# Performance work log

Hardware: AMD Instinct MI355X
Metric: run time of the kernel (lower is better)

The kernel has to match this reference:

```python
import jax, jax.numpy as jnp
import numpy as np

DIM = 512
NUM_HEADS = 8
HEAD_DIM = DIM // NUM_HEADS
REL_POS_BINS = 961
B, N = 64, 256


def setup_inputs() -> dict:
    key = jax.random.key(0)
    ks = jax.random.split(key, 7)
    x = jax.random.normal(ks[0], (B, N, DIM), dtype=jnp.float32)
    rel_pos_index = jax.random.randint(ks[1], (N, N), 0, REL_POS_BINS)
    s = 1.0 / np.sqrt(DIM)
    qkv_w = jax.random.normal(ks[2], (3 * DIM, DIM), dtype=jnp.float32) * s
    qkv_b = jax.random.normal(ks[3], (3 * DIM,), dtype=jnp.float32) * 0.02
    proj_w = jax.random.normal(ks[4], (DIM, DIM), dtype=jnp.float32) * s
    proj_b = jax.random.normal(ks[5], (DIM,), dtype=jnp.float32) * 0.02
    rel_pos_bias = jax.random.normal(ks[6], (NUM_HEADS, REL_POS_BINS), dtype=jnp.float32) * 0.02
    return {"x": x, "rel_pos_index": rel_pos_index, "qkv_w": qkv_w,
            "qkv_b": qkv_b, "proj_w": proj_w, "proj_b": proj_b,
            "rel_pos_bias": rel_pos_bias}


def reference(x, rel_pos_index, qkv_w, qkv_b, proj_w, proj_b, rel_pos_bias):
    Bn, Nn, C = x.shape
    H, D = NUM_HEADS, HEAD_DIM
    qkv = x @ qkv_w.T + qkv_b                      # (B,N,3C)
    qkv = qkv.reshape(Bn, Nn, 3, H, D).transpose(2, 0, 3, 1, 4)  # (3,B,H,N,D)
    q, k, v = qkv[0], qkv[1], qkv[2]
    scale = 1.0 / jnp.sqrt(jnp.asarray(D, dtype=x.dtype))
    scores = jnp.einsum('bhnd,bhmd->bhnm', q, k) * scale          # (B,H,N,N)
    bias = rel_pos_bias[:, rel_pos_index]                          # (H,N,N) gather
    scores = scores + bias[None]
    attn = jax.nn.softmax(scores, axis=-1)
    out = jnp.einsum('bhnm,bhmd->bhnd', attn, v)                   # (B,H,N,D)
    out = out.transpose(0, 2, 1, 3).reshape(Bn, Nn, C)
    return out @ proj_w.T + proj_b
```

## Files before the change

### kernel.cpp

```cpp
#include <hip/hip_runtime.h>
#include <stdint.h>

#define DIM 512
#define NHEADS 8
#define HDIM 64
#define NBINS 961
#define BATCH 64
#define SEQ 256
#define NTOK (BATCH*SEQ)
#define BHND (BATCH*NHEADS*SEQ*HDIM)

using bf16x8 = __attribute__((ext_vector_type(8))) short;
using f32x4  = __attribute__((ext_vector_type(4))) float;

__device__ __forceinline__ unsigned short f2bf(float f) {
  unsigned u = __float_as_uint(f);
  u += 0x7FFF + ((u >> 16) & 1);
  return (unsigned short)(u >> 16);
}

__device__ __forceinline__ void async16(const void* g, void* lds) {
  __builtin_amdgcn_global_load_lds(
      (const __attribute__((address_space(1))) unsigned int*)g,
      (__attribute__((address_space(3))) unsigned int*)lds,
      16, 0, 0);
}


__global__ void cast_kernel(const float* __restrict__ in,
                            unsigned short* __restrict__ out, int n4) {
  int i = blockIdx.x * 256 + threadIdx.x;
  if (i >= n4) return;
  float4 f = reinterpret_cast<const float4*>(in)[i];
  ushort4 o;
  o.x = f2bf(f.x); o.y = f2bf(f.y); o.z = f2bf(f.z); o.w = f2bf(f.w);
  reinterpret_cast<ushort4*>(out)[i] = o;
}

__global__ void bias_kernel(const int* __restrict__ idx,
                            const float* __restrict__ rpb,
                            float* __restrict__ bf) {
  int i = blockIdx.x * 256 + threadIdx.x;
  if (i >= NHEADS * SEQ * SEQ) return;
  int h = i >> 16;
  int r = i & 65535;
  int n = r >> 8, m = r & 255;
  bf[(size_t)h * 65536 + n * 256 + (m & 15) * 16 + (m >> 4)] = rpb[h * NBINS + idx[r]];
}


__device__ __forceinline__ void stage_tile(const unsigned short* __restrict__ A,
                                           const unsigned short* __restrict__ Bw,
                                           char* slot, int T,
                                           int m0, int n0, int t) {
  const int kk = T * 32;
  const int wv64 = (t >> 6) << 6;
#pragma unroll
  for (int i = 0; i < 2; ++i) {
    int c = t + i * 256;
    int row = c >> 2, ch = c & 3;
    int sch = ch ^ ((row >> 1) & 3);
    const unsigned short* ga = A + (size_t)(m0 + row) * 512 + kk + sch * 8;
    async16(ga, slot + (i * 256 + wv64) * 16);
    const unsigned short* gb = Bw + (size_t)(n0 + row) * 512 + kk + sch * 8;
    async16(gb, slot + 8192 + (i * 256 + wv64) * 16);
  }
}

template<int EPI>
__global__ __launch_bounds__(256, 3) void gemm_bt(
    const unsigned short* __restrict__ A,
    const unsigned short* __restrict__ Bw,
    const float* __restrict__ bias,
    void* __restrict__ outp) {
  __shared__ char gsm[49152];
  const int t = threadIdx.x;
  const int lane = t & 63;
  const int l15 = lane & 15, lg = lane >> 4;
  const int m0 = blockIdx.x * 128, n0 = blockIdx.y * 128;
  const int wv = t >> 6;
  const int wm = wv & 1, wn = wv >> 1;

  f32x4 acc[4][4];
  const f32x4 fz = {0.f, 0.f, 0.f, 0.f};
#pragma unroll
  for (int a = 0; a < 4; ++a)
#pragma unroll
    for (int b = 0; b < 4; ++b) acc[a][b] = fz;

  stage_tile(A, Bw, gsm,         0, m0, n0, t);
  stage_tile(A, Bw, gsm + 16384, 1, m0, n0, t);

  int cur = 0;
#pragma unroll 1
  for (int T = 0; T < 16; ++T) {
    if (T < 15) asm volatile("s_waitcnt vmcnt(4)" ::: "memory");
    else        asm volatile("s_waitcnt vmcnt(0)" ::: "memory");
    __builtin_amdgcn_s_barrier();
    __builtin_amdgcn_sched_barrier(0);

    if (T < 14) {
      int dst = cur + 2; if (dst >= 3) dst -= 3;
      stage_tile(A, Bw, gsm + dst * 16384, T + 2, m0, n0, t);
    }
    __builtin_amdgcn_sched_barrier(0);

    char* As = gsm + cur * 16384;
    char* Bs = As + 8192;
    bf16x8 af[4], bfr[4];
#pragma unroll
    for (int x = 0; x < 4; ++x) {
      int ra = wm * 64 + x * 16 + l15;
      af[x]  = *(const bf16x8*)(As + ra * 64 + ((lg ^ ((ra >> 1) & 3)) * 16));
      int rb = wn * 64 + x * 16 + l15;
      bfr[x] = *(const bf16x8*)(Bs + rb * 64 + ((lg ^ ((rb >> 1) & 3)) * 16));
    }
    asm volatile("s_waitcnt lgkmcnt(0)" ::: "memory");
    __builtin_amdgcn_sched_barrier(0);

    __builtin_amdgcn_s_setprio(1);
#pragma unroll
    for (int mi = 0; mi < 4; ++mi)
#pragma unroll
      for (int ni = 0; ni < 4; ++ni)
        acc[mi][ni] = __builtin_amdgcn_mfma_f32_16x16x32_bf16(af[mi], bfr[ni], acc[mi][ni], 0, 0, 0);
    __builtin_amdgcn_s_setprio(0);

    cur = cur + 1; if (cur >= 3) cur -= 3;
  }

#pragma unroll
  for (int mi = 0; mi < 4; ++mi)
#pragma unroll
    for (int ni = 0; ni < 4; ++ni)
#pragma unroll
      for (int r = 0; r < 4; ++r) {
        int row = m0 + wm * 64 + mi * 16 + lg * 4 + r;
        int col = n0 + wn * 64 + ni * 16 + l15;
        float v = acc[mi][ni][r] + bias[col];
        if (EPI == 0) {
          int which = col >> 9, hd = col & 511;
          int b = row >> 8, n = row & 255;
          ((unsigned short*)outp)[(size_t)which * BHND +
              (((size_t)(b * NHEADS + (hd >> 6)) * SEQ + n) * HDIM) + (hd & 63)] = f2bf(v);
        } else {
          ((float*)outp)[(size_t)row * 512 + col] = v;
        }
      }
}


__global__ __launch_bounds__(512, 2) void attn_kernel(
    const unsigned short* __restrict__ qb,
    const unsigned short* __restrict__ kb,
    const unsigned short* __restrict__ vb,
    const float* __restrict__ biasf,
    unsigned short* __restrict__ aout) {
  extern __shared__ char smem[];
  char* k_s = smem;
  char* v_s = smem + 32768;
  const int t = threadIdx.x, lane = t & 63, w = t >> 6;
  const int l15 = lane & 15, lg = lane >> 4;
  char* P_s = smem + w * 4096;
  const int bh = blockIdx.x;
  const int h = bh & 7;
  const int b = bh >> 3;
  const size_t base = (size_t)bh * (SEQ * HDIM);

#pragma unroll
  for (int i = 0; i < 4; ++i) {
    int c = i * 512 + t;
    int row = c >> 3, sl = c & 7;
    bf16x8 val = *(const bf16x8*)(kb + base + (size_t)c * 8);
    *(bf16x8*)(k_s + row * 128 + ((sl * 16) ^ ((row & 7) << 4))) = val;
  }
#pragma unroll
  for (int i = 0; i < 4; ++i) {
    int c = i * 512 + t;
    int key = c >> 3, d0 = (c & 7) * 8;
    bf16x8 val = *(const bf16x8*)(vb + base + (size_t)c * 8);
#pragma unroll
    for (int j = 0; j < 8; ++j) {
      int d = d0 + j;
      int term = (((d & 7) ^ ((d >> 3) & 7)) << 4);
      *(short*)(v_s + d * 512 + ((key * 2) ^ term)) = val[j];
    }
  }
  bf16x8 qa[2][2];
#pragma unroll
  for (int rf = 0; rf < 2; ++rf)
#pragma unroll
    for (int ks = 0; ks < 2; ++ks)
      qa[rf][ks] = *(const bf16x8*)(qb + base + (size_t)(w * 32 + rf * 16 + l15) * 64 + ks * 32 + lg * 8);
  __syncthreads();

  f32x4 accs[2][16];
  const f32x4 fz = {0.f, 0.f, 0.f, 0.f};
#pragma unroll
  for (int a = 0; a < 2; ++a)
#pragma unroll
    for (int c = 0; c < 16; ++c) accs[a][c] = fz;
  __builtin_amdgcn_s_setprio(1);
#pragma unroll
  for (int cf = 0; cf < 16; ++cf) {
    int key = cf * 16 + l15;
#pragma unroll
    for (int ks = 0; ks < 2; ++ks) {
      bf16x8 kf = *(const bf16x8*)(k_s + key * 128 + ((lg * 16 + ks * 64) ^ ((key & 7) << 4)));
      accs[0][cf] = __builtin_amdgcn_mfma_f32_16x16x32_bf16(qa[0][ks], kf, accs[0][cf], 0, 0, 0);
      accs[1][cf] = __builtin_amdgcn_mfma_f32_16x16x32_bf16(qa[1][ks], kf, accs[1][cf], 0, 0, 0);
    }
  }
  __builtin_amdgcn_s_setprio(0);

  const float* bh_ptr = biasf + (size_t)h * 65536;
#pragma unroll
  for (int rf = 0; rf < 2; ++rf)
#pragma unroll
    for (int r = 0; r < 4; ++r) {
      int n = w * 32 + rf * 16 + lg * 4 + r;
      const f32x4* bp = (const f32x4*)(bh_ptr + n * 256 + l15 * 16);
      f32x4 b0 = bp[0], b1 = bp[1], b2 = bp[2], b3 = bp[3];
#pragma unroll
      for (int cf = 0; cf < 16; ++cf) {
        float bb = (cf < 4) ? b0[cf] : (cf < 8) ? b1[cf - 4] : (cf < 12) ? b2[cf - 8] : b3[cf - 12];
        accs[rf][cf][r] = accs[rf][cf][r] * 0.125f + bb;
      }
    }

  float pinv[2][4];
#pragma unroll
  for (int rf = 0; rf < 2; ++rf)
#pragma unroll
    for (int r = 0; r < 4; ++r) {
      float m = -1e30f;
#pragma unroll
      for (int cf = 0; cf < 16; ++cf) m = fmaxf(m, accs[rf][cf][r]);
#pragma unroll
      for (int off = 1; off < 16; off <<= 1) m = fmaxf(m, __shfl_xor(m, off, 64));
      float s = 0.f;
#pragma unroll
      for (int cf = 0; cf < 16; ++cf) {
        float p = __expf(accs[rf][cf][r] - m);
        accs[rf][cf][r] = p;
        s += p;
      }
#pragma unroll
      for (int off = 1; off < 16; off <<= 1) s += __shfl_xor(s, off, 64);
      pinv[rf][r] = 1.0f / s;
    }

  __syncthreads();

  f32x4 acco[2][4];
#pragma unroll
  for (int a = 0; a < 2; ++a)
#pragma unroll
    for (int c2 = 0; c2 < 4; ++c2) acco[a][c2] = fz;

  for (int ch = 0; ch < 4; ++ch) {
#pragma unroll
    for (int rf = 0; rf < 2; ++rf)
#pragma unroll
      for (int cl = 0; cl < 4; ++cl)
#pragma unroll
        for (int r = 0; r < 4; ++r) {
          int rowl = rf * 16 + lg * 4 + r;
          int ml = cl * 16 + l15;
          float p = accs[rf][ch * 4 + cl][r] * pinv[rf][r];
          *(short*)(P_s + rowl * 128 + ((ml * 2) ^ ((rowl & 7) << 4))) = (short)f2bf(p);
        }
#pragma unroll
    for (int ks = 0; ks < 2; ++ks) {
      bf16x8 pa[2];
#pragma unroll
      for (int rf = 0; rf < 2; ++rf) {
        int row = rf * 16 + l15;
        pa[rf] = *(const bf16x8*)(P_s + row * 128 + ((lg * 16 + ks * 64) ^ ((row & 7) << 4)));
      }
      int keyb = (ch * 64 + ks * 32 + lg * 8) * 2;
      __builtin_amdgcn_s_setprio(1);
#pragma unroll
      for (int df = 0; df < 4; ++df) {
        int d = df * 16 + l15;
        int term = (((d & 7) ^ ((d >> 3) & 7)) << 4);
        bf16x8 vf = *(const bf16x8*)(v_s + d * 512 + (keyb ^ term));
        acco[0][df] = __builtin_amdgcn_mfma_f32_16x16x32_bf16(pa[0], vf, acco[0][df], 0, 0, 0);
        acco[1][df] = __builtin_amdgcn_mfma_f32_16x16x32_bf16(pa[1], vf, acco[1][df], 0, 0, 0);
      }
      __builtin_amdgcn_s_setprio(0);
    }
  }

#pragma unroll
  for (int rf = 0; rf < 2; ++rf)
#pragma unroll
    for (int df = 0; df < 4; ++df)
#pragma unroll
      for (int r = 0; r < 4; ++r) {
        int n = w * 32 + rf * 16 + lg * 4 + r;
        int d = df * 16 + l15;
        aout[((size_t)(b * SEQ + n)) * DIM + h * HDIM + d] = f2bf(acco[rf][df][r]);
      }
}


extern "C" void kernel_launch(void* const* d_in, const int* in_sizes, int n_in,
                              void* d_out, int out_size, void* d_ws, size_t ws_size,
                              hipStream_t stream) {
  const float* x      = (const float*)d_in[0];
  const int*   rpi    = (const int*)d_in[1];
  const float* qkv_w  = (const float*)d_in[2];
  const float* qkv_b  = (const float*)d_in[3];
  const float* proj_w = (const float*)d_in[4];
  const float* proj_b = (const float*)d_in[5];
  const float* rpb    = (const float*)d_in[6];

  char* ws = (char*)d_ws;
  unsigned short* xb    = (unsigned short*)ws;
  unsigned short* wqkv  = (unsigned short*)(ws + 16777216);
  unsigned short* wproj = (unsigned short*)(ws + 18350080);
  float*          biasf = (float*)         (ws + 18874368);
  unsigned short* qkvb  = (unsigned short*)(ws + 20971520);
  unsigned short* aoutb = (unsigned short*)(ws + 71303168);

  cast_kernel<<<8192, 256, 0, stream>>>(x, xb, 2097152);
  cast_kernel<<<768, 256, 0, stream>>>(qkv_w, wqkv, 196608);
  cast_kernel<<<256, 256, 0, stream>>>(proj_w, wproj, 65536);
  bias_kernel<<<2048, 256, 0, stream>>>(rpi, rpb, biasf);

  dim3 g1(128, 12);
  gemm_bt<0><<<g1, 256, 0, stream>>>(xb, wqkv, qkv_b, (void*)qkvb);

  attn_kernel<<<512, 512, 65536, stream>>>(qkvb, qkvb + BHND, qkvb + 2 * (size_t)BHND,
                                           biasf, aoutb);

  dim3 g2(128, 4);
  gemm_bt<1><<<g2, 256, 0, stream>>>(aoutb, wproj, proj_b, d_out);
}
```

Baseline: 110.5 us.

## Use 256-row 8-wave GEMM tiles and split attention per query quarter

The GEMM moves to 512-thread blocks with 256xBN tiles, a 64-wide K step with double buffering, staging of B spread across MFMA phases, and a blockIdx remap that groups neighbouring tiles per XCD. The goal is more operand reuse per LDS load and better L2 locality. Attention now runs one block per quarter of the query rows (256 threads, 2048 blocks) to raise parallelism and cut registers per wave. The cost is that each block reloads the full K and V for its head, four times the K/V staging traffic, and the GEMM needs a large LDS allocation that may limit occupancy.

```diff
diff --git a/kernel.cpp b/kernel.cpp
--- a/kernel.cpp
+++ b/kernel.cpp
@@ -49,95 +49,102 @@
 }
 
 
-__device__ __forceinline__ void stage_tile(const unsigned short* __restrict__ A,
-                                           const unsigned short* __restrict__ Bw,
-                                           char* slot, int T,
-                                           int m0, int n0, int t) {
-  const int kk = T * 32;
-  const int wv64 = (t >> 6) << 6;
+__device__ __forceinline__ void stage_half(const unsigned short* __restrict__ X,
+                                           int row0, int kk, char* dst, int t) {
 #pragma unroll
   for (int i = 0; i < 2; ++i) {
-    int c = t + i * 256;
-    int row = c >> 2, ch = c & 3;
-    int sch = ch ^ ((row >> 1) & 3);
-    const unsigned short* ga = A + (size_t)(m0 + row) * 512 + kk + sch * 8;
-    async16(ga, slot + (i * 256 + wv64) * 16);
-    const unsigned short* gb = Bw + (size_t)(n0 + row) * 512 + kk + sch * 8;
-    async16(gb, slot + 8192 + (i * 256 + wv64) * 16);
-  }
-}
-
-template<int EPI>
-__global__ __launch_bounds__(256, 3) void gemm_bt(
+    int q = i * 512 + t;
+    int r = q >> 3, s = q & 7;
+    const unsigned short* src = X + (size_t)(row0 + r) * 512 + kk + ((s ^ (r & 7)) << 3);
+    async16(src, dst + (size_t)(i * 512 + ((t >> 6) << 6)) * 16);
+  }
+}
+
+template<int NBW, int EPI>
+__global__ __launch_bounds__(512) void gemm8p(
     const unsigned short* __restrict__ A,
     const unsigned short* __restrict__ Bw,
     const float* __restrict__ bias,
-    void* __restrict__ outp) {
-  __shared__ char gsm[49152];
+    void* __restrict__ outp, int nbn, int cpx) {
+  extern __shared__ char gsm[];
+  constexpr int BN   = NBW * 64;
+  constexpr int BUF  = 32768 + NBW * 8192;
   const int t = threadIdx.x;
-  const int lane = t & 63;
-  const int l15 = lane & 15, lg = lane >> 4;
-  const int m0 = blockIdx.x * 128, n0 = blockIdx.y * 128;
-  const int wv = t >> 6;
-  const int wm = wv & 1, wn = wv >> 1;
-
-  f32x4 acc[4][4];
+  const int lane = t & 63, l15 = lane & 15, lg = lane >> 4;
+  const int wv = t >> 6, wm = wv & 1, wn = wv >> 1;
+  const int bid = blockIdx.x;
+  const int nid = (bid & 7) * cpx + (bid >> 3);
+  const int m0 = (nid / nbn) * 256, n0 = (nid % nbn) * BN;
+
+  f32x4 acc[8][NBW];
   const f32x4 fz = {0.f, 0.f, 0.f, 0.f};
 #pragma unroll
-  for (int a = 0; a < 4; ++a)
-#pragma unroll
-    for (int b = 0; b < 4; ++b) acc[a][b] = fz;
-
-  stage_tile(A, Bw, gsm,         0, m0, n0, t);
-  stage_tile(A, Bw, gsm + 16384, 1, m0, n0, t);
+  for (int a = 0; a < 8; ++a)
+#pragma unroll
+    for (int b = 0; b < NBW; ++b) acc[a][b] = fz;
+
+  stage_half(A,  m0,       0, gsm,          t);
+  stage_half(A,  m0 + 128, 0, gsm + 16384,  t);
+  stage_half(Bw, n0,       0, gsm + 32768,  t);
+  if (NBW == 4) stage_half(Bw, n0 + 128, 0, gsm + 49152, t);
 
   int cur = 0;
 #pragma unroll 1
-  for (int T = 0; T < 16; ++T) {
-    if (T < 15) asm volatile("s_waitcnt vmcnt(4)" ::: "memory");
-    else        asm volatile("s_waitcnt vmcnt(0)" ::: "memory");
+  for (int T = 0; T < 8; ++T) {
+    char* Ab  = gsm + cur * BUF;
+    char* Bb  = Ab + 32768;
+    char* nxt = gsm + (cur ^ 1) * BUF;
+
     __builtin_amdgcn_s_barrier();
+    if (T < 7) {
+      stage_half(A, m0,       (T + 1) * 64, nxt,         t);
+      stage_half(A, m0 + 128, (T + 1) * 64, nxt + 16384, t);
+      asm volatile("s_waitcnt vmcnt(4)" ::: "memory");
+    } else {
+      asm volatile("s_waitcnt vmcnt(0)" ::: "memory");
+    }
     __builtin_amdgcn_sched_barrier(0);
 
-    if (T < 14) {
-      int dst = cur + 2; if (dst >= 3) dst -= 3;
-      stage_tile(A, Bw, gsm + dst * 16384, T + 2, m0, n0, t);
-    }
-    __builtin_amdgcn_sched_barrier(0);
-
-    char* As = gsm + cur * 16384;
-    char* Bs = As + 8192;
-    bf16x8 af[4], bfr[4];
-#pragma unroll
-    for (int x = 0; x < 4; ++x) {
-      int ra = wm * 64 + x * 16 + l15;
-      af[x]  = *(const bf16x8*)(As + ra * 64 + ((lg ^ ((ra >> 1) & 3)) * 16));
-      int rb = wn * 64 + x * 16 + l15;
-      bfr[x] = *(const bf16x8*)(Bs + rb * 64 + ((lg ^ ((rb >> 1) & 3)) * 16));
-    }
-    asm volatile("s_waitcnt lgkmcnt(0)" ::: "memory");
-    __builtin_amdgcn_sched_barrier(0);
-
-    __builtin_amdgcn_s_setprio(1);
-#pragma unroll
-    for (int mi = 0; mi < 4; ++mi)
-#pragma unroll
-      for (int ni = 0; ni < 4; ++ni)
-        acc[mi][ni] = __builtin_amdgcn_mfma_f32_16x16x32_bf16(af[mi], bfr[ni], acc[mi][ni], 0, 0, 0);
-    __builtin_amdgcn_s_setprio(0);
-
-    cur = cur + 1; if (cur >= 3) cur -= 3;
-  }
-
-#pragma unroll
-  for (int mi = 0; mi < 4; ++mi)
-#pragma unroll
-    for (int ni = 0; ni < 4; ++ni)
+#pragma unroll
+    for (int ph = 0; ph < 4; ++ph) {
+      const int kh = ph >> 1, mh = ph & 1;
+      if (ph == 1 && T < 7) stage_half(Bw, n0, (T + 1) * 64, nxt + 32768, t);
+      if (NBW == 4 && ph == 2 && T < 7) stage_half(Bw, n0 + 128, (T + 1) * 64, nxt + 49152, t);
+
+      const int sw = ((kh * 4 + lg) ^ (l15 & 7)) * 16;
+      bf16x8 av[4], bv[NBW];
+#pragma unroll
+      for (int mi = 0; mi < 4; ++mi)
+        av[mi] = *(const bf16x8*)(Ab + wm * 16384 + (mh * 64 + mi * 16 + l15) * 128 + sw);
+#pragma unroll
+      for (int ni = 0; ni < NBW; ++ni) {
+        int rb = wn * (NBW * 16) + ni * 16 + l15;
+        bv[ni] = *(const bf16x8*)(Bb + (rb >> 7) * 16384 + (rb & 127) * 128 + sw);
+      }
+      asm volatile("s_waitcnt lgkmcnt(0)" ::: "memory");
+      __builtin_amdgcn_sched_barrier(0);
+      __builtin_amdgcn_s_setprio(1);
+#pragma unroll
+      for (int mi = 0; mi < 4; ++mi)
+#pragma unroll
+        for (int ni = 0; ni < NBW; ++ni)
+          acc[mh * 4 + mi][ni] =
+              __builtin_amdgcn_mfma_f32_16x16x32_bf16(av[mi], bv[ni], acc[mh * 4 + mi][ni], 0, 0, 0);
+      __builtin_amdgcn_s_setprio(0);
+      __builtin_amdgcn_sched_barrier(0);
+    }
+    cur ^= 1;
+  }
+
+#pragma unroll
+  for (int MI = 0; MI < 8; ++MI)
+#pragma unroll
+    for (int ni = 0; ni < NBW; ++ni)
 #pragma unroll
       for (int r = 0; r < 4; ++r) {
-        int row = m0 + wm * 64 + mi * 16 + lg * 4 + r;
-        int col = n0 + wn * 64 + ni * 16 + l15;
-        float v = acc[mi][ni][r] + bias[col];
+        int row = m0 + wm * 128 + MI * 16 + lg * 4 + r;
+        int col = n0 + wn * (NBW * 16) + ni * 16 + l15;
+        float v = acc[MI][ni][r] + bias[col];
         if (EPI == 0) {
           int which = col >> 9, hd = col & 511;
           int b = row >> 8, n = row & 255;
@@ -150,7 +157,7 @@
 }
 
 
-__global__ __launch_bounds__(512, 2) void attn_kernel(
+__global__ __launch_bounds__(256) void attn_kernel(
     const unsigned short* __restrict__ qb,
     const unsigned short* __restrict__ kb,
     const unsigned short* __restrict__ vb,
@@ -161,22 +168,24 @@
   char* v_s = smem + 32768;
   const int t = threadIdx.x, lane = t & 63, w = t >> 6;
   const int l15 = lane & 15, lg = lane >> 4;
-  char* P_s = smem + w * 4096;
-  const int bh = blockIdx.x;
+  char* P_s = smem + w * 2048;
+  const int nid = (blockIdx.x & 7) * 256 + (blockIdx.x >> 3);
+  const int bh = nid >> 2, quarter = nid & 3;
   const int h = bh & 7;
   const int b = bh >> 3;
+  const int row0 = quarter * 64 + w * 16;
   const size_t base = (size_t)bh * (SEQ * HDIM);
 
 #pragma unroll
-  for (int i = 0; i < 4; ++i) {
-    int c = i * 512 + t;
+  for (int i = 0; i < 8; ++i) {
+    int c = i * 256 + t;
     int row = c >> 3, sl = c & 7;
     bf16x8 val = *(const bf16x8*)(kb + base + (size_t)c * 8);
     *(bf16x8*)(k_s + row * 128 + ((sl * 16) ^ ((row & 7) << 4))) = val;
   }
 #pragma unroll
-  for (int i = 0; i < 4; ++i) {
-    int c = i * 512 + t;
+  for (int i = 0; i < 8; ++i) {
+    int c = i * 256 + t;
     int key = c >> 3, d0 = (c & 7) * 8;
     bf16x8 val = *(const bf16x8*)(vb + base + (size_t)c * 8);
 #pragma unroll
@@ -186,20 +195,16 @@
       *(short*)(v_s + d * 512 + ((key * 2) ^ term)) = val[j];
     }
   }
-  bf16x8 qa[2][2];
-#pragma unroll
-  for (int rf = 0; rf < 2; ++rf)
-#pragma unroll
-    for (int ks = 0; ks < 2; ++ks)
-      qa[rf][ks] = *(const bf16x8*)(qb + base + (size_t)(w * 32 + rf * 16 + l15) * 64 + ks * 32 + lg * 8);
+  bf16x8 qa[2];
+#pragma unroll
+  for (int ks = 0; ks < 2; ++ks)
+    qa[ks] = *(const bf16x8*)(qb + base + (size_t)(row0 + l15) * 64 + ks * 32 + lg * 8);
   __syncthreads();
 
-  f32x4 accs[2][16];
+  f32x4 accs[16];
   const f32x4 fz = {0.f, 0.f, 0.f, 0.f};
 #pragma unroll
-  for (int a = 0; a < 2; ++a)
-#pragma unroll
-    for (int c = 0; c < 16; ++c) accs[a][c] = fz;
+  for (int c = 0; c < 16; ++c) accs[c] = fz;
   __builtin_amdgcn_s_setprio(1);
 #pragma unroll
   for (int cf = 0; cf < 16; ++cf) {
@@ -207,77 +212,63 @@
 #pragma unroll
     for (int ks = 0; ks < 2; ++ks) {
       bf16x8 kf = *(const bf16x8*)(k_s + key * 128 + ((lg * 16 + ks * 64) ^ ((key & 7) << 4)));
-      accs[0][cf] = __builtin_amdgcn_mfma_f32_16x16x32_bf16(qa[0][ks], kf, accs[0][cf], 0, 0, 0);
-      accs[1][cf] = __builtin_amdgcn_mfma_f32_16x16x32_bf16(qa[1][ks], kf, accs[1][cf], 0, 0, 0);
+      accs[cf] = __builtin_amdgcn_mfma_f32_16x16x32_bf16(qa[ks], kf, accs[cf], 0, 0, 0);
     }
   }
   __builtin_amdgcn_s_setprio(0);
 
   const float* bh_ptr = biasf + (size_t)h * 65536;
 #pragma unroll
-  for (int rf = 0; rf < 2; ++rf)
-#pragma unroll
-    for (int r = 0; r < 4; ++r) {
-      int n = w * 32 + rf * 16 + lg * 4 + r;
-      const f32x4* bp = (const f32x4*)(bh_ptr + n * 256 + l15 * 16);
-      f32x4 b0 = bp[0], b1 = bp[1], b2 = bp[2], b3 = bp[3];
-#pragma unroll
-      for (int cf = 0; cf < 16; ++cf) {
-        float bb = (cf < 4) ? b0[cf] : (cf < 8) ? b1[cf - 4] : (cf < 12) ? b2[cf - 8] : b3[cf - 12];
-        accs[rf][cf][r] = accs[rf][cf][r] * 0.125f + bb;
+  for (int r = 0; r < 4; ++r) {
+    int n = row0 + lg * 4 + r;
+    const f32x4* bp = (const f32x4*)(bh_ptr + n * 256 + l15 * 16);
+    f32x4 b0 = bp[0], b1 = bp[1], b2 = bp[2], b3 = bp[3];
+#pragma unroll
+    for (int cf = 0; cf < 16; ++cf) {
+      float bb = (cf < 4) ? b0[cf] : (cf < 8) ? b1[cf - 4] : (cf < 12) ? b2[cf - 8] : b3[cf - 12];
+      accs[cf][r] = accs[cf][r] * 0.125f + bb;
+    }
+  }
+
+  float pinv[4];
+#pragma unroll
+  for (int r = 0; r < 4; ++r) {
+    float m = -1e30f;
+#pragma unroll
+    for (int cf = 0; cf < 16; ++cf) m = fmaxf(m, accs[cf][r]);
+#pragma unroll
+    for (int off = 1; off < 16; off <<= 1) m = fmaxf(m, __shfl_xor(m, off, 64));
+    float s = 0.f;
+#pragma unroll
+    for (int cf = 0; cf < 16; ++cf) {
+      float p = __expf(accs[cf][r] - m);
+      accs[cf][r] = p;
+      s += p;
+    }
+#pragma unroll
+    for (int off = 1; off < 16; off <<= 1) s += __shfl_xor(s, off, 64);
+    pinv[r] = 1.0f / s;
+  }
+
+  __syncthreads();
+
+  f32x4 acco[4];
+#pragma unroll
+  for (int c2 = 0; c2 < 4; ++c2) acco[c2] = fz;
+
+  for (int ch = 0; ch < 4; ++ch) {
+#pragma unroll
+    for (int cl = 0; cl < 4; ++cl)
+#pragma unroll
+      for (int r = 0; r < 4; ++r) {
+        int rowl = lg * 4 + r;
+        int ml = cl * 16 + l15;
+        float p = accs[ch * 4 + cl][r] * pinv[r];
+        *(short*)(P_s + rowl * 128 + ((ml * 2) ^ ((rowl & 7) << 4))) = (short)f2bf(p);
       }
-    }
-
-  float pinv[2][4];
-#pragma unroll
-  for (int rf = 0; rf < 2; ++rf)
-#pragma unroll
-    for (int r = 0; r < 4; ++r) {
-      float m = -1e30f;
-#pragma unroll
-      for (int cf = 0; cf < 16; ++cf) m = fmaxf(m, accs[rf][cf][r]);
-#pragma unroll
-      for (int off = 1; off < 16; off <<= 1) m = fmaxf(m, __shfl_xor(m, off, 64));
-      float s = 0.f;
-#pragma unroll
-      for (int cf = 0; cf < 16; ++cf) {
-        float p = __expf(accs[rf][cf][r] - m);
-        accs[rf][cf][r] = p;
-        s += p;
-      }
-#pragma unroll
-      for (int off = 1; off < 16; off <<= 1) s += __shfl_xor(s, off, 64);
-      pinv[rf][r] = 1.0f / s;
-    }
-
-  __syncthreads();
-
-  f32x4 acco[2][4];
-#pragma unroll
-  for (int a = 0; a < 2; ++a)
-#pragma unroll
-    for (int c2 = 0; c2 < 4; ++c2) acco[a][c2] = fz;
-
-  for (int ch = 0; ch < 4; ++ch) {
-#pragma unroll
-    for (int rf = 0; rf < 2; ++rf)
-#pragma unroll
-      for (int cl = 0; cl < 4; ++cl)
-#pragma unroll
-        for (int r = 0; r < 4; ++r) {
-          int rowl = rf * 16 + lg * 4 + r;
-          int ml = cl * 16 + l15;
-          float p = accs[rf][ch * 4 + cl][r] * pinv[rf][r];
-          *(short*)(P_s + rowl * 128 + ((ml * 2) ^ ((rowl & 7) << 4))) = (short)f2bf(p);
-        }
 #pragma unroll
     for (int ks = 0; ks < 2; ++ks) {
-      bf16x8 pa[2];
-#pragma unroll
-      for (int rf = 0; rf < 2; ++rf) {
-        int row = rf * 16 + l15;
-        pa[rf] = *(const bf16x8*)(P_s + row * 128 + ((lg * 16 + ks * 64) ^ ((row & 7) << 4)));
-      }
+      bf16x8 pa = *(const bf16x8*)(P_s + l15 * 128 + ((lg * 16 + ks * 64) ^ ((l15 & 7) << 4)));
       int keyb = (ch * 64 + ks * 32 + lg * 8) * 2;
       __builtin_amdgcn_s_setprio(1);
 #pragma unroll
@@ -285,23 +276,20 @@
         int d = df * 16 + l15;
         int term = (((d & 7) ^ ((d >> 3) & 7)) << 4);
         bf16x8 vf = *(const bf16x8*)(v_s + d * 512 + (keyb ^ term));
-        acco[0][df] = __builtin_amdgcn_mfma_f32_16x16x32_bf16(pa[0], vf, acco[0][df], 0, 0, 0);
-        acco[1][df] = __builtin_amdgcn_mfma_f32_16x16x32_bf16(pa[1], vf, acco[1][df], 0, 0, 0);
+        acco[df] = __builtin_amdgcn_mfma_f32_16x16x32_bf16(pa, vf, acco[df], 0, 0, 0);
       }
       __builtin_amdgcn_s_setprio(0);
     }
   }
 
 #pragma unroll
-  for (int rf = 0; rf < 2; ++rf)
-#pragma unroll
-    for (int df = 0; df < 4; ++df)
-#pragma unroll
-      for (int r = 0; r < 4; ++r) {
-        int n = w * 32 + rf * 16 + lg * 4 + r;
-        int d = df * 16 + l15;
-        aout[((size_t)(b * SEQ + n)) * DIM + h * HDIM + d] = f2bf(acco[rf][df][r]);
-      }
+  for (int df = 0; df < 4; ++df)
+#pragma unroll
+    for (int r = 0; r < 4; ++r) {
+      int n = row0 + lg * 4 + r;
+      int d = df * 16 + l15;
+      aout[((size_t)(b * SEQ + n)) * DIM + h * HDIM + d] = f2bf(acco[df][r]);
+    }
 }
 
 
@@ -329,12 +317,10 @@
   cast_kernel<<<256, 256, 0, stream>>>(proj_w, wproj, 65536);
   bias_kernel<<<2048, 256, 0, stream>>>(rpi, rpb, biasf);
 
-  dim3 g1(128, 12);
-  gemm_bt<0><<<g1, 256, 0, stream>>>(xb, wqkv, qkv_b, (void*)qkvb);
-
-  attn_kernel<<<512, 512, 65536, stream>>>(qkvb, qkvb + BHND, qkvb + 2 * (size_t)BHND,
-                                           biasf, aoutb);
-
-  dim3 g2(128, 4);
-  gemm_bt<1><<<g2, 256, 0, stream>>>(aoutb, wproj, proj_b, d_out);
-}
+  gemm8p<4, 0><<<384, 512, 131072, stream>>>(xb, wqkv, qkv_b, (void*)qkvb, 6, 48);
+
+  attn_kernel<<<2048, 256, 65536, stream>>>(qkvb, qkvb + BHND, qkvb + 2 * (size_t)BHND,
+                                            biasf, aoutb);
+
+  gemm8p<2, 1><<<256, 512, 98304, stream>>>(aoutb, wproj, proj_b, d_out, 4, 32);
+}
```

After: 108.6 us. No clear change (-1.8%).
